# Kernel optimization log

Hardware: AMD Instinct MI355X
Metric: run time of the kernel (lower is better)

## Reference

```python
import jax, jax.numpy as jnp
import numpy as np

B, T, NH, HD = 2, 2048, 12, 128
HIDDEN = NH * HD
EPS = 1.1920928955078125e-07  # torch fp32 finfo eps (F.rms_norm default)


def _rope_cos_sin(T, d_half, base=10000.0):
    inv = 1.0 / (base ** (jnp.arange(d_half, dtype=jnp.float32) / d_half))
    t = jnp.arange(T, dtype=jnp.float32)
    f = t[:, None] * inv[None, :]  # [T, d_half]
    return jnp.cos(f)[None, :, None, :], jnp.sin(f)[None, :, None, :]


def apply_rotary_emb(x, cos, sin):
    d = x.shape[3] // 2
    x1, x2 = x[..., :d], x[..., d:]
    return jnp.concatenate([x1 * cos + x2 * sin, x1 * -sin + x2 * cos], axis=3)


def rms_norm(x):
    return x * jax.lax.rsqrt(jnp.mean(x * x, axis=-1, keepdims=True) + EPS)


def setup_inputs() -> dict:
    key = jax.random.key(0)
    ks = jax.random.split(key, 5)
    x = jax.random.normal(ks[0], (B, T, HIDDEN), dtype=jnp.float32)
    cos, sin = _rope_cos_sin(T, HD // 2)
    s = 1.0 / np.sqrt(HIDDEN)
    Wq = jax.random.normal(ks[1], (HIDDEN, HIDDEN), dtype=jnp.float32) * s
    Wk = jax.random.normal(ks[2], (HIDDEN, HIDDEN), dtype=jnp.float32) * s
    Wv = jax.random.normal(ks[3], (HIDDEN, HIDDEN), dtype=jnp.float32) * s
    Wp = jax.random.normal(ks[4], (HIDDEN, HIDDEN), dtype=jnp.float32) * s
    return {"x": x, "cos": cos, "sin": sin, "Wq": Wq, "Wk": Wk, "Wv": Wv,
            "Wp": Wp, "window": 1024}


def reference(x, cos, sin, Wq, Wk, Wv, Wp, window):
    Bx, Tx, _ = x.shape
    q = (x @ Wq.T).reshape(Bx, Tx, NH, HD)
    k = (x @ Wk.T).reshape(Bx, Tx, NH, HD)
    v = (x @ Wv.T).reshape(Bx, Tx, NH, HD)
    q = rms_norm(apply_rotary_emb(q, cos, sin))
    k = rms_norm(apply_rotary_emb(k, cos, sin))
    # causal + sliding-window attention (dense, matching the sdpa fallback)
    scale = 1.0 / np.sqrt(HD)
    scores = jnp.einsum('bqhd,bkhd->bhqk', q, k) * scale
    row = jnp.arange(Tx)[:, None]
    col = jnp.arange(Tx)[None, :]
    mask = (col <= row) & (row - col <= window)
    scores = jnp.where(mask[None, None], scores, jnp.finfo(scores.dtype).min)
    attn = jax.nn.softmax(scores, axis=-1)
    y = jnp.einsum('bhqk,bkhd->bqhd', attn, v).reshape(Bx, Tx, HIDDEN)
    return y @ Wp.T
```

## Files before the change

kernel.cpp:

```cpp
#include <hip/hip_runtime.h>
#include <stdint.h>

#define HIDDEN 1536
#define NHEAD 12
#define HD 128
#define TSEQ 2048
#define NROWS 4096
#define KDIM HIDDEN
#define EPS_F 1.1920928955078125e-07f
#define SCALE_LOG2E 0.12751879110195655f
#define FIXSUB 16.6f

typedef unsigned short u16;
typedef __bf16 bf16x8_t __attribute__((ext_vector_type(8)));
typedef float f32x4_t __attribute__((ext_vector_type(4)));

#define MFMA16(a, b, c) __builtin_amdgcn_mfma_f32_16x16x32_bf16((a), (b), (c), 0, 0, 0)

__device__ __forceinline__ u16 f2bf(float f) {
  unsigned u = __builtin_bit_cast(unsigned, f);
  u = (u + 0x7fffu + ((u >> 16) & 1u)) >> 16;
  return (u16)u;
}
__device__ __forceinline__ float bfu(u16 v) {
  return __builtin_bit_cast(float, ((unsigned)v) << 16);
}

__global__ __launch_bounds__(256) void cast_kernel(const float* __restrict__ in,
                                                   u16* __restrict__ out, int n) {
  int i = (blockIdx.x * 256 + threadIdx.x) * 4;
  if (i >= n) return;
  float4 v = *reinterpret_cast<const float4*>(in + i);
  uint2 pk;
  pk.x = (unsigned)f2bf(v.x) | ((unsigned)f2bf(v.y) << 16);
  pk.y = (unsigned)f2bf(v.z) | ((unsigned)f2bf(v.w) << 16);
  *reinterpret_cast<uint2*>(out + i) = pk;
}

__global__ __launch_bounds__(256) void cast4_kernel(
    const float* __restrict__ a, const float* __restrict__ b, const float* __restrict__ c,
    const float* __restrict__ d, u16* __restrict__ oa, u16* __restrict__ ob,
    u16* __restrict__ oc, u16* __restrict__ od, int n) {
  const float* in;
  u16* out;
  switch (blockIdx.y) {
    case 0: in = a; out = oa; break;
    case 1: in = b; out = ob; break;
    case 2: in = c; out = oc; break;
    default: in = d; out = od; break;
  }
  int i = (blockIdx.x * 256 + threadIdx.x) * 4;
  if (i >= n) return;
  float4 v = *reinterpret_cast<const float4*>(in + i);
  uint2 pk;
  pk.x = (unsigned)f2bf(v.x) | ((unsigned)f2bf(v.y) << 16);
  pk.y = (unsigned)f2bf(v.z) | ((unsigned)f2bf(v.w) << 16);
  *reinterpret_cast<uint2*>(out + i) = pk;
}

__device__ __forceinline__ void gemm_mainloop(const u16* __restrict__ A,
                                              const u16* __restrict__ W, int M0, int N0,
                                              u16* lds, f32x4_t acc[4][4], int tid) {
  const int w = tid >> 6, l = tid & 63;
  const int lrow = l & 15, kg = l >> 4;
  const int wr = (w >> 1) * 64, wc = (w & 1) * 64;
  const int c0 = w * 128 + l;
  const int c1 = c0 + 64;
  const u16* pa0 = A + (size_t)(M0 + (c0 >> 2)) * KDIM + (c0 & 3) * 8;
  const u16* pa1 = A + (size_t)(M0 + (c1 >> 2)) * KDIM + (c1 & 3) * 8;
  const u16* pw0 = W + (size_t)(N0 + (c0 >> 2)) * KDIM + (c0 & 3) * 8;
  const u16* pw1 = W + (size_t)(N0 + (c1 >> 2)) * KDIM + (c1 & 3) * 8;
  u16* dA = lds + w * 1024;
  u16* dW = lds + 8192 + w * 1024;
  auto issue = [&](int buf) {
    __builtin_amdgcn_global_load_lds((const __attribute__((address_space(1))) void*)pa0,
        (__attribute__((address_space(3))) void*)(dA + buf * 4096), 16, 0, 0);
    __builtin_amdgcn_global_load_lds((const __attribute__((address_space(1))) void*)pa1,
        (__attribute__((address_space(3))) void*)(dA + buf * 4096 + 512), 16, 0, 0);
    __builtin_amdgcn_global_load_lds((const __attribute__((address_space(1))) void*)pw0,
        (__attribute__((address_space(3))) void*)(dW + buf * 4096), 16, 0, 0);
    __builtin_amdgcn_global_load_lds((const __attribute__((address_space(1))) void*)pw1,
        (__attribute__((address_space(3))) void*)(dW + buf * 4096 + 512), 16, 0, 0);
    pa0 += 32; pa1 += 32; pw0 += 32; pw1 += 32;
  };
  issue(0);
  const int NT = KDIM / 32;
#pragma unroll 1
  for (int kt = 0; kt < NT; ++kt) {
    const int cur = kt & 1;
    if (kt + 1 < NT) {
      issue(cur ^ 1);
      asm volatile("s_waitcnt vmcnt(4)" ::: "memory");
    } else {
      asm volatile("s_waitcnt vmcnt(0)" ::: "memory");
    }
    __builtin_amdgcn_s_barrier();
    asm volatile("" ::: "memory");
    const u16* Ab = lds + cur * 4096;
    const u16* Wb = lds + 8192 + cur * 4096;
    bf16x8_t af[4], bf_[4];
#pragma unroll
    for (int m = 0; m < 4; ++m)
      af[m] = *reinterpret_cast<const bf16x8_t*>(Ab + (wr + m * 16 + lrow) * 32 + kg * 8);
#pragma unroll
    for (int n = 0; n < 4; ++n)
      bf_[n] = *reinterpret_cast<const bf16x8_t*>(Wb + (wc + n * 16 + lrow) * 32 + kg * 8);
#pragma unroll
    for (int m = 0; m < 4; ++m)
#pragma unroll
      for (int n = 0; n < 4; ++n)
        acc[m][n] = MFMA16(af[m], bf_[n], acc[m][n]);
    asm volatile("s_waitcnt lgkmcnt(0)" ::: "memory");
    __builtin_amdgcn_s_barrier();
    asm volatile("" ::: "memory");
  }
}

__global__ __launch_bounds__(256) void gemm_qkv_kernel(
    const u16* __restrict__ xb, const u16* __restrict__ wq, const u16* __restrict__ wk,
    const u16* __restrict__ wv, const float* __restrict__ cosp, const float* __restrict__ sinp,
    u16* __restrict__ qh, u16* __restrict__ kh, u16* __restrict__ vt) {
  __shared__ __align__(16) u16 lds[16384];
  const int tid = threadIdx.x;
  const int wgid = blockIdx.x;
  const int xcd = wgid & 7, c = wgid >> 3;
  const int m = ((xcd & 3) << 3) + (c & 7);
  const int nz = ((xcd >> 2) * 18) + (c >> 3);
  const int z = nz / 12, n = nz % 12;
  const int M0 = m * 128, N0 = n * 128;
  const u16* W = (z == 0) ? wq : (z == 1) ? wk : wv;
  f32x4_t acc[4][4] = {};
  gemm_mainloop(xb, W, M0, N0, lds, acc, tid);
  const int w = tid >> 6, l = tid & 63;
  const int lrow = l & 15, kg = l >> 4;
  const int wr = (w >> 1) * 64, wc = (w & 1) * 64;
  char* cs = reinterpret_cast<char*>(lds);
  if (z == 2) {
#pragma unroll
    for (int mi = 0; mi < 4; ++mi)
#pragma unroll
      for (int ni = 0; ni < 4; ++ni)
#pragma unroll
        for (int r = 0; r < 4; ++r) {
          const int t_l = wr + mi * 16 + kg * 4 + r;
          const int d = wc + ni * 16 + lrow;
          const int bofs = (d * 256 + t_l * 2) ^ ((d & 7) << 4);
          *reinterpret_cast<u16*>(cs + bofs) = f2bf(acc[mi][ni][r]);
        }
  } else {
#pragma unroll
    for (int mi = 0; mi < 4; ++mi)
#pragma unroll
      for (int ni = 0; ni < 4; ++ni)
#pragma unroll
        for (int r = 0; r < 4; ++r) {
          const int t_l = wr + mi * 16 + kg * 4 + r;
          const int d = wc + ni * 16 + lrow;
          const int bofs = (t_l * 256 + d * 2) ^ ((t_l & 7) << 4);
          *reinterpret_cast<u16*>(cs + bofs) = f2bf(acc[mi][ni][r]);
        }
  }
  __syncthreads();
  const int rr = tid >> 1, hh = tid & 1;
  const int bb = M0 >> 11;
  const int t0 = M0 & (TSEQ - 1);
  const size_t bhn = (size_t)(bb * NHEAD + n);
  if (z == 2) {
    u16* dst = vt + (bhn * HD + rr) * TSEQ + t0 + hh * 64;
    const char* base = cs + rr * 256 + hh * 128;
#pragma unroll
    for (int j = 0; j < 8; ++j) {
      uint4 v = *reinterpret_cast<const uint4*>(base + ((j ^ (rr & 7)) * 16));
      *reinterpret_cast<uint4*>(dst + j * 8) = v;
    }
  } else {
    const int t = (t0 + rr);
    const float* cosb = cosp + t * 64;
    const float* sinb = sinp + t * 64;
    const char* base = cs + rr * 256;
    float ss = 0.0f;
    unsigned pk[32];
#pragma unroll
    for (int j = 0; j < 8; ++j) {
      const int jp = (j ^ (rr & 7)) * 16;
      uint4 vo = *reinterpret_cast<const uint4*>(base + hh * 128 + jp);
      uint4 vx = *reinterpret_cast<const uint4*>(base + (hh ^ 1) * 128 + jp);
      const unsigned vo32[4] = {vo.x, vo.y, vo.z, vo.w};
      const unsigned vx32[4] = {vx.x, vx.y, vx.z, vx.w};
      const float* cj = cosb + j * 8;
      const float* sj = sinb + j * 8;
#pragma unroll
      for (int q2 = 0; q2 < 4; ++q2) {
        float o0 = bfu((u16)(vo32[q2] & 0xffffu)), o1 = bfu((u16)(vo32[q2] >> 16));
        float x0 = bfu((u16)(vx32[q2] & 0xffffu)), x1 = bfu((u16)(vx32[q2] >> 16));
        float c0 = cj[q2 * 2], c1 = cj[q2 * 2 + 1];
        float s0 = sj[q2 * 2], s1 = sj[q2 * 2 + 1];
        float y0 = hh ? __builtin_fmaf(o0, c0, -x0 * s0) : __builtin_fmaf(o0, c0, x0 * s0);
        float y1 = hh ? __builtin_fmaf(o1, c1, -x1 * s1) : __builtin_fmaf(o1, c1, x1 * s1);
        ss = __builtin_fmaf(y0, y0, __builtin_fmaf(y1, y1, ss));
        pk[j * 4 + q2] = (unsigned)f2bf(y0) | ((unsigned)f2bf(y1) << 16);
      }
    }
    ss += __shfl_xor(ss, 1, 64);
    const float rinv = rsqrtf(ss * (1.0f / 128.0f) + EPS_F);
    u16* dst = ((z == 0) ? qh : kh) + (bhn * TSEQ + t) * HD + hh * 64;
#pragma unroll
    for (int j = 0; j < 8; ++j) {
      unsigned o[4];
#pragma unroll
      for (int q2 = 0; q2 < 4; ++q2) {
        float y0 = bfu((u16)(pk[j * 4 + q2] & 0xffffu)) * rinv;
        float y1 = bfu((u16)(pk[j * 4 + q2] >> 16)) * rinv;
        o[q2] = (unsigned)f2bf(y0) | ((unsigned)f2bf(y1) << 16);
      }
      uint4 v;
      v.x = o[0]; v.y = o[1]; v.z = o[2]; v.w = o[3];
      *reinterpret_cast<uint4*>(dst + j * 8) = v;
    }
  }
}

__global__ __launch_bounds__(256) void gemm_out_kernel(const u16* __restrict__ yh,
                                                       const u16* __restrict__ wp,
                                                       float* __restrict__ out) {
  __shared__ __align__(16) u16 lds[16384];
  const int tid = threadIdx.x;
  const int wgid = blockIdx.x;
  const int xcd = wgid & 7, c = wgid >> 3;
  const int m = ((xcd & 3) << 3) + (c & 7);
  const int n = ((xcd >> 2) * 6) + (c >> 3);
  const int M0 = m * 128, N0 = n * 128;
  f32x4_t acc[4][4] = {};
  gemm_mainloop(yh, wp, M0, N0, lds, acc, tid);
  const int w = tid >> 6, l = tid & 63;
  const int lrow = l & 15, kg = l >> 4;
  const int wr = (w >> 1) * 64, wc = (w & 1) * 64;
#pragma unroll
  for (int mi = 0; mi < 4; ++mi)
#pragma unroll
    for (int ni = 0; ni < 4; ++ni)
#pragma unroll
      for (int r = 0; r < 4; ++r) {
        const int grow = M0 + wr + mi * 16 + kg * 4 + r;
        const int gcol = N0 + wc + ni * 16 + lrow;
        out[(size_t)grow * HIDDEN + gcol] = acc[mi][ni][r];
      }
}

__global__ __launch_bounds__(256, 2) void attn_kernel(const u16* __restrict__ qh,
                                                      const u16* __restrict__ kh,
                                                      const u16* __restrict__ vt,
                                                      u16* __restrict__ yh,
                                                      const int* __restrict__ winp) {
  __shared__ __align__(16) u16 Kl[2][8192];
  __shared__ __align__(16) u16 Vl[8192];
  __shared__ __align__(16) u16 Pl[4][1024];
  const int tid = threadIdx.x, w = tid >> 6, l = tid & 63;
  const int lrow = l & 15, kg = l >> 4;
  const int bid = blockIdx.x;
  const int swz = (bid & 7) * 96 + (bid >> 3);
  const int qb = swz & 31;
  const int bh = swz >> 5;
  const int h = bh % NHEAD, b = bh / NHEAD;
  const int win = winp[0];
  const u16* Q = qh + (size_t)bh * TSEQ * HD;
  const u16* K = kh + (size_t)bh * TSEQ * HD;
  const u16* V = vt + (size_t)bh * HD * TSEQ;
  const int qw = qb * 64 + w * 16;
  bf16x8_t aq[4];
#pragma unroll
  for (int ks = 0; ks < 4; ++ks)
    aq[ks] = *reinterpret_cast<const bf16x8_t*>(Q + (qw + lrow) * HD + ks * 32 + kg * 8);
  float lrun[4] = {0.f, 0.f, 0.f, 0.f};
  f32x4_t accv[8] = {};
  int lo = qb * 64 - win;
  if (lo < 0) lo = 0;
  lo &= ~63;
  const int last = qb * 64;
  u16* Pw = &Pl[w][0];

  auto stage_k = [&](int kv, int buf) {
#pragma unroll
    for (int i = 0; i < 4; ++i) {
      const int c = i * 256 + w * 64 + l;
      const int row = c >> 4, j = c & 15;
      const u16* src = K + (size_t)(kv + row) * HD + ((j ^ (row & 7)) * 8);
      __builtin_amdgcn_global_load_lds(
          (const __attribute__((address_space(1))) void*)src,
          (__attribute__((address_space(3))) void*)(&Kl[buf][0] + i * 2048 + w * 512), 16, 0, 0);
    }
  };
  auto stage_v = [&](int kv) {
#pragma unroll
    for (int i = 0; i < 4; ++i) {
      const int c = i * 256 + w * 64 + l;
      const int row = c >> 3, j = c & 7;
      const u16* src = V + (size_t)row * TSEQ + kv + ((j ^ (row & 7)) * 8);
      __builtin_amdgcn_global_load_lds(
          (const __attribute__((address_space(1))) void*)src,
          (__attribute__((address_space(3))) void*)(&Vl[0] + i * 2048 + w * 512), 16, 0, 0);
    }
  };

  stage_k(lo, 0);
  int it = 0;
  for (int kv = lo; kv <= last; kv += 64, ++it) {
    const int cur = it & 1;
    stage_v(kv);
    stage_k(kv + 64, cur ^ 1);
    asm volatile("s_waitcnt vmcnt(8)" ::: "memory");
    __builtin_amdgcn_s_barrier();
    asm volatile("" ::: "memory");
    const u16* Kb = &Kl[cur][0];
    f32x4_t s[4] = {};
#pragma unroll
    for (int n = 0; n < 4; ++n) {
      const int row = n * 16 + lrow;
#pragma unroll
      for (int ks = 0; ks < 4; ++ks) {
        bf16x8_t bk = *reinterpret_cast<const bf16x8_t*>(
            Kb + row * 128 + (((ks << 2) | kg) ^ (row & 7)) * 8);
        s[n] = MFMA16(aq[ks], bk, s[n]);
      }
    }
    float ps[4][4];
    float psum[4];
#pragma unroll
    for (int n = 0; n < 4; ++n) {
      const int key = kv + n * 16 + lrow;
#pragma unroll
      for (int r = 0; r < 4; ++r) {
        const int rowq = qw + kg * 4 + r;
        const bool ok = (key <= rowq) && (rowq - key <= win);
        ps[n][r] = ok ? exp2f(__builtin_fmaf(s[n][r], SCALE_LOG2E, -FIXSUB)) : 0.0f;
      }
    }
#pragma unroll
    for (int r = 0; r < 4; ++r) psum[r] = (ps[0][r] + ps[1][r]) + (ps[2][r] + ps[3][r]);
#pragma unroll
    for (int off = 1; off < 16; off <<= 1)
#pragma unroll
      for (int r = 0; r < 4; ++r) psum[r] += __shfl_xor(psum[r], off, 64);
#pragma unroll
    for (int r = 0; r < 4; ++r) lrun[r] += psum[r];
#pragma unroll
    for (int n = 0; n < 4; ++n)
#pragma unroll
      for (int r = 0; r < 4; ++r) {
        const int rp = kg * 4 + r;
        int bofs = rp * 128 + (n * 16 + lrow) * 2;
        bofs ^= (rp & 7) << 4;
        *reinterpret_cast<u16*>(reinterpret_cast<char*>(Pw) + bofs) = f2bf(ps[n][r]);
      }
    asm volatile("s_waitcnt lgkmcnt(0)" ::: "memory");
    asm volatile("s_waitcnt vmcnt(4)" ::: "memory");
    __builtin_amdgcn_s_barrier();
    asm volatile("" ::: "memory");
    bf16x8_t ap[2];
#pragma unroll
    for (int k2 = 0; k2 < 2; ++k2) {
      int bofs = lrow * 128 + k2 * 64 + kg * 16;
      bofs ^= (lrow & 7) << 4;
      ap[k2] = *reinterpret_cast<const bf16x8_t*>(reinterpret_cast<const char*>(Pw) + bofs);
    }
#pragma unroll
    for (int k2 = 0; k2 < 2; ++k2)
#pragma unroll
      for (int dn = 0; dn < 8; ++dn) {
        const int row = dn * 16 + lrow;
        bf16x8_t bv = *reinterpret_cast<const bf16x8_t*>(
            Vl + row * 64 + (((k2 << 2) | kg) ^ (row & 7)) * 8);
        accv[dn] = MFMA16(ap[k2], bv, accv[dn]);
      }
    __builtin_amdgcn_s_barrier();
    asm volatile("" ::: "memory");
  }
  float inv[4];
#pragma unroll
  for (int r = 0; r < 4; ++r) inv[r] = 1.0f / lrun[r];
#pragma unroll
  for (int dn = 0; dn < 8; ++dn)
#pragma unroll
    for (int r = 0; r < 4; ++r) {
      const int rowg = b * TSEQ + qw + kg * 4 + r;
      const int col = h * HD + dn * 16 + lrow;
      yh[(size_t)rowg * HIDDEN + col] = f2bf(accv[dn][r] * inv[r]);
    }
}

extern "C" void kernel_launch(void* const* d_in, const int* in_sizes, int n_in, void* d_out,
                              int out_size, void* d_ws, size_t ws_size, hipStream_t stream) {
  const float* x = (const float*)d_in[0];
  const float* cosp = (const float*)d_in[1];
  const float* sinp = (const float*)d_in[2];
  const float* Wq = (const float*)d_in[3];
  const float* Wk = (const float*)d_in[4];
  const float* Wv = (const float*)d_in[5];
  const float* Wp = (const float*)d_in[6];
  const int* winp = (const int*)d_in[7];

  char* ws = (char*)d_ws;
  size_t off = 0;
  auto alloc = [&](size_t bytes) {
    char* p = ws + off;
    off += (bytes + 255) & ~(size_t)255;
    return p;
  };
  u16* xb = (u16*)alloc((size_t)NROWS * HIDDEN * 2);
  u16* wqb = (u16*)alloc((size_t)HIDDEN * HIDDEN * 2);
  u16* wkb = (u16*)alloc((size_t)HIDDEN * HIDDEN * 2);
  u16* wvb = (u16*)alloc((size_t)HIDDEN * HIDDEN * 2);
  u16* wpb = (u16*)alloc((size_t)HIDDEN * HIDDEN * 2);
  u16* qh = (u16*)alloc((size_t)NROWS * HIDDEN * 2);
  u16* kh = (u16*)alloc((size_t)NROWS * HIDDEN * 2);
  u16* vt = (u16*)alloc((size_t)NROWS * HIDDEN * 2);
  u16* yh = (u16*)alloc((size_t)NROWS * HIDDEN * 2);

  const int nx = NROWS * HIDDEN;
  const int nw = HIDDEN * HIDDEN;
  cast_kernel<<<nx / 1024, 256, 0, stream>>>(x, xb, nx);
  cast4_kernel<<<dim3(nw / 1024, 4), 256, 0, stream>>>(Wq, Wk, Wv, Wp, wqb, wkb, wvb, wpb, nw);

  gemm_qkv_kernel<<<dim3(1152), 256, 0, stream>>>(xb, wqb, wkb, wvb, cosp, sinp, qh, kh, vt);
  attn_kernel<<<dim3(768), 256, 0, stream>>>(qh, kh, vt, yh, winp);
  gemm_out_kernel<<<dim3(384), 256, 0, stream>>>(yh, wpb, (float*)d_out);
}
```

Baseline: 212.2 us.

## Fuse Q/K/V projections into one GEMM tile sharing the x tile

The QKV GEMM now computes all three projections (Q, K, V) for the same 128x128 output tile in one workgroup. Each staged tile of x is reused across the three weight matrices, cutting x loads and the grid from 1152 to 384 workgroups. In exchange, the accumulator state triples (192 fp32 values per lane) and LDS grows to 64 KB, which risks register pressure or spills and lowers occupancy and latency hiding with fewer blocks. The epilogue runs the RoPE/RMSNorm and transpose passes sequentially for each projection.

```diff
diff --git a/kernel.cpp b/kernel.cpp
--- a/kernel.cpp
+++ b/kernel.cpp
@@ -16,6 +16,9 @@
 typedef float f32x4_t __attribute__((ext_vector_type(4)));
 
 #define MFMA16(a, b, c) __builtin_amdgcn_mfma_f32_16x16x32_bf16((a), (b), (c), 0, 0, 0)
+#define GLL(srcp, dstp) \
+  __builtin_amdgcn_global_load_lds((const __attribute__((address_space(1))) void*)(srcp), \
+                                   (__attribute__((address_space(3))) void*)(dstp), 16, 0, 0)
 
 __device__ __forceinline__ u16 f2bf(float f) {
   unsigned u = __builtin_bit_cast(unsigned, f);
@@ -58,6 +61,164 @@
   *reinterpret_cast<uint2*>(out + i) = pk;
 }
 
+__global__ __launch_bounds__(256, 2) void gemm_qkv_kernel(
+    const u16* __restrict__ xb, const u16* __restrict__ wq, const u16* __restrict__ wk,
+    const u16* __restrict__ wv, const float* __restrict__ cosp, const float* __restrict__ sinp,
+    u16* __restrict__ qh, u16* __restrict__ kh, u16* __restrict__ vt) {
+  __shared__ __align__(16) u16 lds[32768];
+  const int tid = threadIdx.x;
+  const int wgid = blockIdx.x;
+  const int xcd = wgid & 7, c = wgid >> 3;
+  const int m = ((xcd & 3) << 3) + (c & 7);
+  const int n = ((xcd >> 2) * 6) + (c >> 3);
+  const int M0 = m * 128, N0 = n * 128;
+  const int w = tid >> 6, l = tid & 63;
+  const int lrow = l & 15, kg = l >> 4;
+  const int wr = (w >> 1) * 64, wc = (w & 1) * 64;
+  const int c0 = w * 128 + l;
+  const int c1 = c0 + 64;
+  unsigned offA0 = (unsigned)((M0 + (c0 >> 2)) * KDIM + (c0 & 3) * 8);
+  unsigned offA1 = (unsigned)((M0 + (c1 >> 2)) * KDIM + (c1 & 3) * 8);
+  unsigned offW0 = (unsigned)((N0 + (c0 >> 2)) * KDIM + (c0 & 3) * 8);
+  unsigned offW1 = (unsigned)((N0 + (c1 >> 2)) * KDIM + (c1 & 3) * 8);
+  f32x4_t acc[3][4][4] = {};
+  auto issue = [&](int buf) {
+    u16* bb = lds + buf * 16384 + w * 1024;
+    GLL(xb + offA0, bb);
+    GLL(xb + offA1, bb + 512);
+    GLL(wq + offW0, bb + 4096);
+    GLL(wq + offW1, bb + 4096 + 512);
+    GLL(wk + offW0, bb + 8192);
+    GLL(wk + offW1, bb + 8192 + 512);
+    GLL(wv + offW0, bb + 12288);
+    GLL(wv + offW1, bb + 12288 + 512);
+    offA0 += 32; offA1 += 32; offW0 += 32; offW1 += 32;
+  };
+  issue(0);
+  const int NT = KDIM / 32;
+#pragma unroll 1
+  for (int kt = 0; kt < NT; ++kt) {
+    const int cur = kt & 1;
+    if (kt + 1 < NT) {
+      issue(cur ^ 1);
+      asm volatile("s_waitcnt vmcnt(8)" ::: "memory");
+    } else {
+      asm volatile("s_waitcnt vmcnt(0)" ::: "memory");
+    }
+    __builtin_amdgcn_s_barrier();
+    asm volatile("" ::: "memory");
+    const u16* Ab = lds + cur * 16384;
+    bf16x8_t af[4];
+#pragma unroll
+    for (int mi = 0; mi < 4; ++mi)
+      af[mi] = *reinterpret_cast<const bf16x8_t*>(Ab + (wr + mi * 16 + lrow) * 32 + kg * 8);
+#pragma unroll
+    for (int z = 0; z < 3; ++z) {
+      const u16* Wb = Ab + 4096 + z * 4096;
+      bf16x8_t bf_[4];
+#pragma unroll
+      for (int ni = 0; ni < 4; ++ni)
+        bf_[ni] = *reinterpret_cast<const bf16x8_t*>(Wb + (wc + ni * 16 + lrow) * 32 + kg * 8);
+#pragma unroll
+      for (int mi = 0; mi < 4; ++mi)
+#pragma unroll
+        for (int ni = 0; ni < 4; ++ni)
+          acc[z][mi][ni] = MFMA16(af[mi], bf_[ni], acc[z][mi][ni]);
+    }
+    asm volatile("s_waitcnt lgkmcnt(0)" ::: "memory");
+    __builtin_amdgcn_s_barrier();
+    asm volatile("" ::: "memory");
+  }
+  char* cs = reinterpret_cast<char*>(lds);
+  const int rr = tid >> 1, hh = tid & 1;
+  const int bb2 = M0 >> 11;
+  const int t0 = M0 & (TSEQ - 1);
+  const size_t bhn = (size_t)(bb2 * NHEAD + n);
+#pragma unroll
+  for (int z = 0; z < 3; ++z) {
+    if (z == 2) {
+#pragma unroll
+      for (int mi = 0; mi < 4; ++mi)
+#pragma unroll
+        for (int ni = 0; ni < 4; ++ni)
+#pragma unroll
+          for (int r = 0; r < 4; ++r) {
+            const int t_l = wr + mi * 16 + kg * 4 + r;
+            const int d = wc + ni * 16 + lrow;
+            const int bofs = (d * 256 + t_l * 2) ^ ((d & 7) << 4);
+            *reinterpret_cast<u16*>(cs + bofs) = f2bf(acc[z][mi][ni][r]);
+          }
+    } else {
+#pragma unroll
+      for (int mi = 0; mi < 4; ++mi)
+#pragma unroll
+        for (int ni = 0; ni < 4; ++ni)
+#pragma unroll
+          for (int r = 0; r < 4; ++r) {
+            const int t_l = wr + mi * 16 + kg * 4 + r;
+            const int d = wc + ni * 16 + lrow;
+            const int bofs = (t_l * 256 + d * 2) ^ ((t_l & 7) << 4);
+            *reinterpret_cast<u16*>(cs + bofs) = f2bf(acc[z][mi][ni][r]);
+          }
+    }
+    __syncthreads();
+    if (z == 2) {
+      u16* dst = vt + (bhn * HD + rr) * TSEQ + t0 + hh * 64;
+      const char* base = cs + rr * 256 + hh * 128;
+#pragma unroll
+      for (int j = 0; j < 8; ++j) {
+        uint4 v = *reinterpret_cast<const uint4*>(base + ((j ^ (rr & 7)) * 16));
+        *reinterpret_cast<uint4*>(dst + j * 8) = v;
+      }
+    } else {
+      const int t = t0 + rr;
+      const float* cosb = cosp + t * 64;
+      const float* sinb = sinp + t * 64;
+      const char* base = cs + rr * 256;
+      float ss = 0.0f;
+      unsigned pk[32];
+#pragma unroll
+      for (int j = 0; j < 8; ++j) {
+        const int jp = (j ^ (rr & 7)) * 16;
+        uint4 vo = *reinterpret_cast<const uint4*>(base + hh * 128 + jp);
+        uint4 vx = *reinterpret_cast<const uint4*>(base + (hh ^ 1) * 128 + jp);
+        const unsigned vo32[4] = {vo.x, vo.y, vo.z, vo.w};
+        const unsigned vx32[4] = {vx.x, vx.y, vx.z, vx.w};
+        const float* cj = cosb + j * 8;
+        const float* sj = sinb + j * 8;
+#pragma unroll
+        for (int q2 = 0; q2 < 4; ++q2) {
+          float o0 = bfu((u16)(vo32[q2] & 0xffffu)), o1 = bfu((u16)(vo32[q2] >> 16));
+          float x0 = bfu((u16)(vx32[q2] & 0xffffu)), x1 = bfu((u16)(vx32[q2] >> 16));
+          float cc0 = cj[q2 * 2], cc1 = cj[q2 * 2 + 1];
+          float s0 = sj[q2 * 2], s1 = sj[q2 * 2 + 1];
+          float y0 = hh ? __builtin_fmaf(o0, cc0, -x0 * s0) : __builtin_fmaf(o0, cc0, x0 * s0);
+          float y1 = hh ? __builtin_fmaf(o1, cc1, -x1 * s1) : __builtin_fmaf(o1, cc1, x1 * s1);
+          ss = __builtin_fmaf(y0, y0, __builtin_fmaf(y1, y1, ss));
+          pk[j * 4 + q2] = (unsigned)f2bf(y0) | ((unsigned)f2bf(y1) << 16);
+        }
+      }
+      ss += __shfl_xor(ss, 1, 64);
+      const float rinv = rsqrtf(ss * (1.0f / 128.0f) + EPS_F);
+      u16* dst = ((z == 0) ? qh : kh) + (bhn * TSEQ + t) * HD + hh * 64;
+#pragma unroll
+      for (int j = 0; j < 8; ++j) {
+        unsigned o[4];
+#pragma unroll
+        for (int q2 = 0; q2 < 4; ++q2) {
+          float y0 = bfu((u16)(pk[j * 4 + q2] & 0xffffu)) * rinv;
+          float y1 = bfu((u16)(pk[j * 4 + q2] >> 16)) * rinv;
+          o[q2] = (unsigned)f2bf(y0) | ((unsigned)f2bf(y1) << 16);
+        }
+        uint4 v;
+        v.x = o[0]; v.y = o[1]; v.z = o[2]; v.w = o[3];
+        *reinterpret_cast<uint4*>(dst + j * 8) = v;
+      }
+    }
+    __syncthreads();
+  }
+}
+
 __device__ __forceinline__ void gemm_mainloop(const u16* __restrict__ A,
                                               const u16* __restrict__ W, int M0, int N0,
                                               u16* lds, f32x4_t acc[4][4], int tid) {
@@ -73,14 +234,10 @@
   u16* dA = lds + w * 1024;
   u16* dW = lds + 8192 + w * 1024;
   auto issue = [&](int buf) {
-    __builtin_amdgcn_global_load_lds((const __attribute__((address_space(1))) void*)pa0,
-        (__attribute__((address_space(3))) void*)(dA + buf * 4096), 16, 0, 0);
-    __builtin_amdgcn_global_load_lds((const __attribute__((address_space(1))) void*)pa1,
-        (__attribute__((address_space(3))) void*)(dA + buf * 4096 + 512), 16, 0, 0);
-    __builtin_amdgcn_global_load_lds((const __attribute__((address_space(1))) void*)pw0,
-        (__attribute__((address_space(3))) void*)(dW + buf * 4096), 16, 0, 0);
-    __builtin_amdgcn_global_load_lds((const __attribute__((address_space(1))) void*)pw1,
-        (__attribute__((address_space(3))) void*)(dW + buf * 4096 + 512), 16, 0, 0);
+    GLL(pa0, dA + buf * 4096);
+    GLL(pa1, dA + buf * 4096 + 512);
+    GLL(pw0, dW + buf * 4096);
+    GLL(pw1, dW + buf * 4096 + 512);
     pa0 += 32; pa1 += 32; pw0 += 32; pw1 += 32;
   };
   issue(0);
@@ -100,123 +257,19 @@
     const u16* Wb = lds + 8192 + cur * 4096;
     bf16x8_t af[4], bf_[4];
 #pragma unroll
-    for (int m = 0; m < 4; ++m)
-      af[m] = *reinterpret_cast<const bf16x8_t*>(Ab + (wr + m * 16 + lrow) * 32 + kg * 8);
-#pragma unroll
-    for (int n = 0; n < 4; ++n)
-      bf_[n] = *reinterpret_cast<const bf16x8_t*>(Wb + (wc + n * 16 + lrow) * 32 + kg * 8);
-#pragma unroll
-    for (int m = 0; m < 4; ++m)
-#pragma unroll
-      for (int n = 0; n < 4; ++n)
-        acc[m][n] = MFMA16(af[m], bf_[n], acc[m][n]);
+    for (int mi = 0; mi < 4; ++mi)
+      af[mi] = *reinterpret_cast<const bf16x8_t*>(Ab + (wr + mi * 16 + lrow) * 32 + kg * 8);
+#pragma unroll
+    for (int ni = 0; ni < 4; ++ni)
+      bf_[ni] = *reinterpret_cast<const bf16x8_t*>(Wb + (wc + ni * 16 + lrow) * 32 + kg * 8);
+#pragma unroll
+    for (int mi = 0; mi < 4; ++mi)
+#pragma unroll
+      for (int ni = 0; ni < 4; ++ni)
+        acc[mi][ni] = MFMA16(af[mi], bf_[ni], acc[mi][ni]);
     asm volatile("s_waitcnt lgkmcnt(0)" ::: "memory");
     __builtin_amdgcn_s_barrier();
     asm volatile("" ::: "memory");
-  }
-}
-
-__global__ __launch_bounds__(256) void gemm_qkv_kernel(
-    const u16* __restrict__ xb, const u16* __restrict__ wq, const u16* __restrict__ wk,
-    const u16* __restrict__ wv, const float* __restrict__ cosp, const float* __restrict__ sinp,
-    u16* __restrict__ qh, u16* __restrict__ kh, u16* __restrict__ vt) {
-  __shared__ __align__(16) u16 lds[16384];
-  const int tid = threadIdx.x;
-  const int wgid = blockIdx.x;
-  const int xcd = wgid & 7, c = wgid >> 3;
-  const int m = ((xcd & 3) << 3) + (c & 7);
-  const int nz = ((xcd >> 2) * 18) + (c >> 3);
-  const int z = nz / 12, n = nz % 12;
-  const int M0 = m * 128, N0 = n * 128;
-  const u16* W = (z == 0) ? wq : (z == 1) ? wk : wv;
-  f32x4_t acc[4][4] = {};
-  gemm_mainloop(xb, W, M0, N0, lds, acc, tid);
-  const int w = tid >> 6, l = tid & 63;
-  const int lrow = l & 15, kg = l >> 4;
-  const int wr = (w >> 1) * 64, wc = (w & 1) * 64;
-  char* cs = reinterpret_cast<char*>(lds);
-  if (z == 2) {
-#pragma unroll
-    for (int mi = 0; mi < 4; ++mi)
-#pragma unroll
-      for (int ni = 0; ni < 4; ++ni)
-#pragma unroll
-        for (int r = 0; r < 4; ++r) {
-          const int t_l = wr + mi * 16 + kg * 4 + r;
-          const int d = wc + ni * 16 + lrow;
-          const int bofs = (d * 256 + t_l * 2) ^ ((d & 7) << 4);
-          *reinterpret_cast<u16*>(cs + bofs) = f2bf(acc[mi][ni][r]);
-        }
-  } else {
-#pragma unroll
-    for (int mi = 0; mi < 4; ++mi)
-#pragma unroll
-      for (int ni = 0; ni < 4; ++ni)
-#pragma unroll
-        for (int r = 0; r < 4; ++r) {
-          const int t_l = wr + mi * 16 + kg * 4 + r;
-          const int d = wc + ni * 16 + lrow;
-          const int bofs = (t_l * 256 + d * 2) ^ ((t_l & 7) << 4);
-          *reinterpret_cast<u16*>(cs + bofs) = f2bf(acc[mi][ni][r]);
-        }
-  }
-  __syncthreads();
-  const int rr = tid >> 1, hh = tid & 1;
-  const int bb = M0 >> 11;
-  const int t0 = M0 & (TSEQ - 1);
-  const size_t bhn = (size_t)(bb * NHEAD + n);
-  if (z == 2) {
-    u16* dst = vt + (bhn * HD + rr) * TSEQ + t0 + hh * 64;
-    const char* base = cs + rr * 256 + hh * 128;
-#pragma unroll
-    for (int j = 0; j < 8; ++j) {
-      uint4 v = *reinterpret_cast<const uint4*>(base + ((j ^ (rr & 7)) * 16));
-      *reinterpret_cast<uint4*>(dst + j * 8) = v;
-    }
-  } else {
-    const int t = (t0 + rr);
-    const float* cosb = cosp + t * 64;
-    const float* sinb = sinp + t * 64;
-    const char* base = cs + rr * 256;
-    float ss = 0.0f;
-    unsigned pk[32];
-#pragma unroll
-    for (int j = 0; j < 8; ++j) {
-      const int jp = (j ^ (rr & 7)) * 16;
-      uint4 vo = *reinterpret_cast<const uint4*>(base + hh * 128 + jp);
-      uint4 vx = *reinterpret_cast<const uint4*>(base + (hh ^ 1) * 128 + jp);
-      const unsigned vo32[4] = {vo.x, vo.y, vo.z, vo.w};
-      const unsigned vx32[4] = {vx.x, vx.y, vx.z, vx.w};
-      const float* cj = cosb + j * 8;
-      const float* sj = sinb + j * 8;
-#pragma unroll
-      for (int q2 = 0; q2 < 4; ++q2) {
-        float o0 = bfu((u16)(vo32[q2] & 0xffffu)), o1 = bfu((u16)(vo32[q2] >> 16));
-        float x0 = bfu((u16)(vx32[q2] & 0xffffu)), x1 = bfu((u16)(vx32[q2] >> 16));
-        float c0 = cj[q2 * 2], c1 = cj[q2 * 2 + 1];
-        float s0 = sj[q2 * 2], s1 = sj[q2 * 2 + 1];
-        float y0 = hh ? __builtin_fmaf(o0, c0, -x0 * s0) : __builtin_fmaf(o0, c0, x0 * s0);
-        float y1 = hh ? __builtin_fmaf(o1, c1, -x1 * s1) : __builtin_fmaf(o1, c1, x1 * s1);
-        ss = __builtin_fmaf(y0, y0, __builtin_fmaf(y1, y1, ss));
-        pk[j * 4 + q2] = (unsigned)f2bf(y0) | ((unsigned)f2bf(y1) << 16);
-      }
-    }
-    ss += __shfl_xor(ss, 1, 64);
-    const float rinv = rsqrtf(ss * (1.0f / 128.0f) + EPS_F);
-    u16* dst = ((z == 0) ? qh : kh) + (bhn * TSEQ + t) * HD + hh * 64;
-#pragma unroll
-    for (int j = 0; j < 8; ++j) {
-      unsigned o[4];
-#pragma unroll
-      for (int q2 = 0; q2 < 4; ++q2) {
-        float y0 = bfu((u16)(pk[j * 4 + q2] & 0xffffu)) * rinv;
-        float y1 = bfu((u16)(pk[j * 4 + q2] >> 16)) * rinv;
-        o[q2] = (unsigned)f2bf(y0) | ((unsigned)f2bf(y1) << 16);
-      }
-      uint4 v;
-      v.x = o[0]; v.y = o[1]; v.z = o[2]; v.w = o[3];
-      *reinterpret_cast<uint4*>(dst + j * 8) = v;
-    }
   }
 }
 
@@ -285,9 +338,7 @@
       const int c = i * 256 + w * 64 + l;
       const int row = c >> 4, j = c & 15;
       const u16* src = K + (size_t)(kv + row) * HD + ((j ^ (row & 7)) * 8);
-      __builtin_amdgcn_global_load_lds(
-          (const __attribute__((address_space(1))) void*)src,
-          (__attribute__((address_space(3))) void*)(&Kl[buf][0] + i * 2048 + w * 512), 16, 0, 0);
+      GLL(src, &Kl[buf][0] + i * 2048 + w * 512);
     }
   };
   auto stage_v = [&](int kv) {
@@ -296,9 +347,7 @@
       const int c = i * 256 + w * 64 + l;
       const int row = c >> 3, j = c & 7;
       const u16* src = V + (size_t)row * TSEQ + kv + ((j ^ (row & 7)) * 8);
-      __builtin_amdgcn_global_load_lds(
-          (const __attribute__((address_space(1))) void*)src,
-          (__attribute__((address_space(3))) void*)(&Vl[0] + i * 2048 + w * 512), 16, 0, 0);
+      GLL(src, &Vl[0] + i * 2048 + w * 512);
     }
   };
 
@@ -421,7 +470,7 @@
   cast_kernel<<<nx / 1024, 256, 0, stream>>>(x, xb, nx);
   cast4_kernel<<<dim3(nw / 1024, 4), 256, 0, stream>>>(Wq, Wk, Wv, Wp, wqb, wkb, wvb, wpb, nw);
 
-  gemm_qkv_kernel<<<dim3(1152), 256, 0, stream>>>(xb, wqb, wkb, wvb, cosp, sinp, qh, kh, vt);
+  gemm_qkv_kernel<<<dim3(384), 256, 0, stream>>>(xb, wqb, wkb, wvb, cosp, sinp, qh, kh, vt);
   attn_kernel<<<dim3(768), 256, 0, stream>>>(qh, kh, vt, yh, winp);
   gemm_out_kernel<<<dim3(384), 256, 0, stream>>>(yh, wpb, (float*)d_out);
 }
```

Measured after the change: 250.4 us. +18.0%, slower.

## Deepen GEMM K-tile to 64 with swizzled LDS and enlarge attention query blocks

Applied to the files above, without the earlier changes.

The shared GEMM mainloop now stages 64-wide K tiles instead of 32, with an XOR-swizzled LDS layout and double buffering. This halves the number of barrier round-trips and doubles the LDS footprint. The attention kernel moves from 4 to 8 waves per block, covering 128 queries per block, so each K/V tile staged in LDS is reused by twice as many query rows. The cost is more LDS per block, a different occupancy target, and extra KV iterations for the block that sits on the causal diagonal.

```diff
diff --git a/kernel.cpp b/kernel.cpp
--- a/kernel.cpp
+++ b/kernel.cpp
@@ -16,6 +16,9 @@
 typedef float f32x4_t __attribute__((ext_vector_type(4)));
 
 #define MFMA16(a, b, c) __builtin_amdgcn_mfma_f32_16x16x32_bf16((a), (b), (c), 0, 0, 0)
+#define GLL(srcp, dstp) \
+  __builtin_amdgcn_global_load_lds((const __attribute__((address_space(1))) void*)(srcp), \
+                                   (__attribute__((address_space(3))) void*)(dstp), 16, 0, 0)
 
 __device__ __forceinline__ u16 f2bf(float f) {
   unsigned u = __builtin_bit_cast(unsigned, f);
@@ -58,58 +61,63 @@
   *reinterpret_cast<uint2*>(out + i) = pk;
 }
 
-__device__ __forceinline__ void gemm_mainloop(const u16* __restrict__ A,
-                                              const u16* __restrict__ W, int M0, int N0,
-                                              u16* lds, f32x4_t acc[4][4], int tid) {
+__device__ __forceinline__ void gemm_mainloop64(const u16* __restrict__ A,
+                                                const u16* __restrict__ W, int M0, int N0,
+                                                u16* lds, f32x4_t acc[4][4], int tid) {
   const int w = tid >> 6, l = tid & 63;
   const int lrow = l & 15, kg = l >> 4;
   const int wr = (w >> 1) * 64, wc = (w & 1) * 64;
-  const int c0 = w * 128 + l;
-  const int c1 = c0 + 64;
-  const u16* pa0 = A + (size_t)(M0 + (c0 >> 2)) * KDIM + (c0 & 3) * 8;
-  const u16* pa1 = A + (size_t)(M0 + (c1 >> 2)) * KDIM + (c1 & 3) * 8;
-  const u16* pw0 = W + (size_t)(N0 + (c0 >> 2)) * KDIM + (c0 & 3) * 8;
-  const u16* pw1 = W + (size_t)(N0 + (c1 >> 2)) * KDIM + (c1 & 3) * 8;
-  u16* dA = lds + w * 1024;
-  u16* dW = lds + 8192 + w * 1024;
+  const int row0 = tid >> 3, j0 = tid & 7;
+  const unsigned jsw = (unsigned)((j0 ^ (row0 & 7)) * 8);
+  unsigned offA = (unsigned)((M0 + row0) * KDIM) + jsw;
+  unsigned offW = (unsigned)((N0 + row0) * KDIM) + jsw;
+  const u16* A1 = A + 32 * KDIM; const u16* A2 = A + 64 * KDIM; const u16* A3 = A + 96 * KDIM;
+  const u16* W1 = W + 32 * KDIM; const u16* W2 = W + 64 * KDIM; const u16* W3 = W + 96 * KDIM;
   auto issue = [&](int buf) {
-    __builtin_amdgcn_global_load_lds((const __attribute__((address_space(1))) void*)pa0,
-        (__attribute__((address_space(3))) void*)(dA + buf * 4096), 16, 0, 0);
-    __builtin_amdgcn_global_load_lds((const __attribute__((address_space(1))) void*)pa1,
-        (__attribute__((address_space(3))) void*)(dA + buf * 4096 + 512), 16, 0, 0);
-    __builtin_amdgcn_global_load_lds((const __attribute__((address_space(1))) void*)pw0,
-        (__attribute__((address_space(3))) void*)(dW + buf * 4096), 16, 0, 0);
-    __builtin_amdgcn_global_load_lds((const __attribute__((address_space(1))) void*)pw1,
-        (__attribute__((address_space(3))) void*)(dW + buf * 4096 + 512), 16, 0, 0);
-    pa0 += 32; pa1 += 32; pw0 += 32; pw1 += 32;
+    u16* da = lds + buf * 8192 + w * 512;
+    u16* dw = lds + 16384 + buf * 8192 + w * 512;
+    GLL(A + offA, da);          GLL(A1 + offA, da + 2048);
+    GLL(A2 + offA, da + 4096);  GLL(A3 + offA, da + 6144);
+    GLL(W + offW, dw);          GLL(W1 + offW, dw + 2048);
+    GLL(W2 + offW, dw + 4096);  GLL(W3 + offW, dw + 6144);
+    offA += 64; offW += 64;
   };
   issue(0);
-  const int NT = KDIM / 32;
+  const int NT = KDIM / 64;
 #pragma unroll 1
   for (int kt = 0; kt < NT; ++kt) {
     const int cur = kt & 1;
     if (kt + 1 < NT) {
       issue(cur ^ 1);
-      asm volatile("s_waitcnt vmcnt(4)" ::: "memory");
+      asm volatile("s_waitcnt vmcnt(8)" ::: "memory");
     } else {
       asm volatile("s_waitcnt vmcnt(0)" ::: "memory");
     }
     __builtin_amdgcn_s_barrier();
     asm volatile("" ::: "memory");
-    const u16* Ab = lds + cur * 4096;
-    const u16* Wb = lds + 8192 + cur * 4096;
-    bf16x8_t af[4], bf_[4];
-#pragma unroll
-    for (int m = 0; m < 4; ++m)
-      af[m] = *reinterpret_cast<const bf16x8_t*>(Ab + (wr + m * 16 + lrow) * 32 + kg * 8);
-#pragma unroll
-    for (int n = 0; n < 4; ++n)
-      bf_[n] = *reinterpret_cast<const bf16x8_t*>(Wb + (wc + n * 16 + lrow) * 32 + kg * 8);
-#pragma unroll
-    for (int m = 0; m < 4; ++m)
-#pragma unroll
-      for (int n = 0; n < 4; ++n)
-        acc[m][n] = MFMA16(af[m], bf_[n], acc[m][n]);
+    const u16* Ab = lds + cur * 8192;
+    const u16* Wb = lds + 16384 + cur * 8192;
+#pragma unroll
+    for (int s = 0; s < 2; ++s) {
+      bf16x8_t af[4], bf_[4];
+#pragma unroll
+      for (int mi = 0; mi < 4; ++mi) {
+        const int row = wr + mi * 16 + lrow;
+        af[mi] = *reinterpret_cast<const bf16x8_t*>(Ab + row * 64 +
+                                                    (((s << 2) | kg) ^ (row & 7)) * 8);
+      }
+#pragma unroll
+      for (int ni = 0; ni < 4; ++ni) {
+        const int row = wc + ni * 16 + lrow;
+        bf_[ni] = *reinterpret_cast<const bf16x8_t*>(Wb + row * 64 +
+                                                     (((s << 2) | kg) ^ (row & 7)) * 8);
+      }
+#pragma unroll
+      for (int mi = 0; mi < 4; ++mi)
+#pragma unroll
+        for (int ni = 0; ni < 4; ++ni)
+          acc[mi][ni] = MFMA16(af[mi], bf_[ni], acc[mi][ni]);
+    }
     asm volatile("s_waitcnt lgkmcnt(0)" ::: "memory");
     __builtin_amdgcn_s_barrier();
     asm volatile("" ::: "memory");
@@ -120,7 +128,7 @@
     const u16* __restrict__ xb, const u16* __restrict__ wq, const u16* __restrict__ wk,
     const u16* __restrict__ wv, const float* __restrict__ cosp, const float* __restrict__ sinp,
     u16* __restrict__ qh, u16* __restrict__ kh, u16* __restrict__ vt) {
-  __shared__ __align__(16) u16 lds[16384];
+  __shared__ __align__(16) u16 lds[32768];
   const int tid = threadIdx.x;
   const int wgid = blockIdx.x;
   const int xcd = wgid & 7, c = wgid >> 3;
@@ -130,7 +138,7 @@
   const int M0 = m * 128, N0 = n * 128;
   const u16* W = (z == 0) ? wq : (z == 1) ? wk : wv;
   f32x4_t acc[4][4] = {};
-  gemm_mainloop(xb, W, M0, N0, lds, acc, tid);
+  gemm_mainloop64(xb, W, M0, N0, lds, acc, tid);
   const int w = tid >> 6, l = tid & 63;
   const int lrow = l & 15, kg = l >> 4;
   const int wr = (w >> 1) * 64, wc = (w & 1) * 64;
@@ -174,7 +182,7 @@
       *reinterpret_cast<uint4*>(dst + j * 8) = v;
     }
   } else {
-    const int t = (t0 + rr);
+    const int t = t0 + rr;
     const float* cosb = cosp + t * 64;
     const float* sinb = sinp + t * 64;
     const char* base = cs + rr * 256;
@@ -193,10 +201,10 @@
       for (int q2 = 0; q2 < 4; ++q2) {
         float o0 = bfu((u16)(vo32[q2] & 0xffffu)), o1 = bfu((u16)(vo32[q2] >> 16));
         float x0 = bfu((u16)(vx32[q2] & 0xffffu)), x1 = bfu((u16)(vx32[q2] >> 16));
-        float c0 = cj[q2 * 2], c1 = cj[q2 * 2 + 1];
+        float cc0 = cj[q2 * 2], cc1 = cj[q2 * 2 + 1];
         float s0 = sj[q2 * 2], s1 = sj[q2 * 2 + 1];
-        float y0 = hh ? __builtin_fmaf(o0, c0, -x0 * s0) : __builtin_fmaf(o0, c0, x0 * s0);
-        float y1 = hh ? __builtin_fmaf(o1, c1, -x1 * s1) : __builtin_fmaf(o1, c1, x1 * s1);
+        float y0 = hh ? __builtin_fmaf(o0, cc0, -x0 * s0) : __builtin_fmaf(o0, cc0, x0 * s0);
+        float y1 = hh ? __builtin_fmaf(o1, cc1, -x1 * s1) : __builtin_fmaf(o1, cc1, x1 * s1);
         ss = __builtin_fmaf(y0, y0, __builtin_fmaf(y1, y1, ss));
         pk[j * 4 + q2] = (unsigned)f2bf(y0) | ((unsigned)f2bf(y1) << 16);
       }
@@ -223,7 +231,7 @@
 __global__ __launch_bounds__(256) void gemm_out_kernel(const u16* __restrict__ yh,
                                                        const u16* __restrict__ wp,
                                                        float* __restrict__ out) {
-  __shared__ __align__(16) u16 lds[16384];
+  __shared__ __align__(16) u16 lds[32768];
   const int tid = threadIdx.x;
   const int wgid = blockIdx.x;
   const int xcd = wgid & 7, c = wgid >> 3;
@@ -231,7 +239,7 @@
   const int n = ((xcd >> 2) * 6) + (c >> 3);
   const int M0 = m * 128, N0 = n * 128;
   f32x4_t acc[4][4] = {};
-  gemm_mainloop(yh, wp, M0, N0, lds, acc, tid);
+  gemm_mainloop64(yh, wp, M0, N0, lds, acc, tid);
   const int w = tid >> 6, l = tid & 63;
   const int lrow = l & 15, kg = l >> 4;
   const int wr = (w >> 1) * 64, wc = (w & 1) * 64;
@@ -247,58 +255,54 @@
       }
 }
 
-__global__ __launch_bounds__(256, 2) void attn_kernel(const u16* __restrict__ qh,
+__global__ __launch_bounds__(512, 4) void attn_kernel(const u16* __restrict__ qh,
                                                       const u16* __restrict__ kh,
                                                       const u16* __restrict__ vt,
                                                       u16* __restrict__ yh,
                                                       const int* __restrict__ winp) {
   __shared__ __align__(16) u16 Kl[2][8192];
   __shared__ __align__(16) u16 Vl[8192];
-  __shared__ __align__(16) u16 Pl[4][1024];
+  __shared__ __align__(16) u16 Pl[8][1024];
   const int tid = threadIdx.x, w = tid >> 6, l = tid & 63;
   const int lrow = l & 15, kg = l >> 4;
   const int bid = blockIdx.x;
-  const int swz = (bid & 7) * 96 + (bid >> 3);
-  const int qb = swz & 31;
-  const int bh = swz >> 5;
+  const int swz = (bid & 7) * 48 + (bid >> 3);
+  const int qb = swz & 15;
+  const int bh = swz >> 4;
   const int h = bh % NHEAD, b = bh / NHEAD;
   const int win = winp[0];
   const u16* Q = qh + (size_t)bh * TSEQ * HD;
   const u16* K = kh + (size_t)bh * TSEQ * HD;
   const u16* V = vt + (size_t)bh * HD * TSEQ;
-  const int qw = qb * 64 + w * 16;
+  const int qw = qb * 128 + w * 16;
   bf16x8_t aq[4];
 #pragma unroll
   for (int ks = 0; ks < 4; ++ks)
     aq[ks] = *reinterpret_cast<const bf16x8_t*>(Q + (qw + lrow) * HD + ks * 32 + kg * 8);
   float lrun[4] = {0.f, 0.f, 0.f, 0.f};
   f32x4_t accv[8] = {};
-  int lo = qb * 64 - win;
+  int lo = qb * 128 - win;
   if (lo < 0) lo = 0;
   lo &= ~63;
-  const int last = qb * 64;
+  const int last = qb * 128 + 64;
   u16* Pw = &Pl[w][0];
 
   auto stage_k = [&](int kv, int buf) {
 #pragma unroll
-    for (int i = 0; i < 4; ++i) {
-      const int c = i * 256 + w * 64 + l;
+    for (int i = 0; i < 2; ++i) {
+      const int c = i * 512 + w * 64 + l;
       const int row = c >> 4, j = c & 15;
       const u16* src = K + (size_t)(kv + row) * HD + ((j ^ (row & 7)) * 8);
-      __builtin_amdgcn_global_load_lds(
-          (const __attribute__((address_space(1))) void*)src,
-          (__attribute__((address_space(3))) void*)(&Kl[buf][0] + i * 2048 + w * 512), 16, 0, 0);
+      GLL(src, &Kl[buf][0] + i * 4096 + w * 512);
     }
   };
   auto stage_v = [&](int kv) {
 #pragma unroll
-    for (int i = 0; i < 4; ++i) {
-      const int c = i * 256 + w * 64 + l;
+    for (int i = 0; i < 2; ++i) {
+      const int c = i * 512 + w * 64 + l;
       const int row = c >> 3, j = c & 7;
       const u16* src = V + (size_t)row * TSEQ + kv + ((j ^ (row & 7)) * 8);
-      __builtin_amdgcn_global_load_lds(
-          (const __attribute__((address_space(1))) void*)src,
-          (__attribute__((address_space(3))) void*)(&Vl[0] + i * 2048 + w * 512), 16, 0, 0);
+      GLL(src, &Vl[0] + i * 4096 + w * 512);
     }
   };
 
@@ -308,7 +312,7 @@
     const int cur = it & 1;
     stage_v(kv);
     stage_k(kv + 64, cur ^ 1);
-    asm volatile("s_waitcnt vmcnt(8)" ::: "memory");
+    asm volatile("s_waitcnt vmcnt(4)" ::: "memory");
     __builtin_amdgcn_s_barrier();
     asm volatile("" ::: "memory");
     const u16* Kb = &Kl[cur][0];
@@ -353,7 +357,7 @@
         *reinterpret_cast<u16*>(reinterpret_cast<char*>(Pw) + bofs) = f2bf(ps[n][r]);
       }
     asm volatile("s_waitcnt lgkmcnt(0)" ::: "memory");
-    asm volatile("s_waitcnt vmcnt(4)" ::: "memory");
+    asm volatile("s_waitcnt vmcnt(2)" ::: "memory");
     __builtin_amdgcn_s_barrier();
     asm volatile("" ::: "memory");
     bf16x8_t ap[2];
@@ -422,6 +426,6 @@
   cast4_kernel<<<dim3(nw / 1024, 4), 256, 0, stream>>>(Wq, Wk, Wv, Wp, wqb, wkb, wvb, wpb, nw);
 
   gemm_qkv_kernel<<<dim3(1152), 256, 0, stream>>>(xb, wqb, wkb, wvb, cosp, sinp, qh, kh, vt);
-  attn_kernel<<<dim3(768), 256, 0, stream>>>(qh, kh, vt, yh, winp);
+  attn_kernel<<<dim3(384), 512, 0, stream>>>(qh, kh, vt, yh, winp);
   gemm_out_kernel<<<dim3(384), 256, 0, stream>>>(yh, wpb, (float*)d_out);
 }
```

After: 196.8 us. 1.08x faster.
